# Performance work log

Hardware: AMD Instinct MI355X
Metric: run time of the kernel (lower is better)

## Reference

```python
import jax, jax.numpy as jnp
import numpy as np

D_MODEL, D_FF, N_EXPERTS, TOP_K = 1024, 4096, 8, 2


def setup_inputs() -> dict:
    key = jax.random.key(0)
    ks = jax.random.split(key, 7)
    s = 0.02
    return {
        "x": jax.random.normal(ks[0], (2, 2048, D_MODEL), dtype=jnp.float32),
        "router_w": jax.random.normal(ks[1], (D_MODEL, N_EXPERTS), dtype=jnp.float32) * s,
        "router_b": jnp.zeros((N_EXPERTS,), dtype=jnp.float32),
        "w1": jax.random.normal(ks[2], (N_EXPERTS, D_MODEL, D_FF), dtype=jnp.float32) * s,
        "b1": jnp.zeros((N_EXPERTS, D_FF), dtype=jnp.float32),
        "w2": jax.random.normal(ks[3], (N_EXPERTS, D_FF, D_MODEL), dtype=jnp.float32) * s,
        "b2": jnp.zeros((N_EXPERTS, D_MODEL), dtype=jnp.float32),
    }


def reference(x, router_w, router_b, w1, b1, w2, b2):
    bsz, seq_len, d_model = x.shape
    flat_x = x.reshape(-1, d_model)                      # [T, D]
    logits = flat_x @ router_w + router_b                # [T, E]
    topk_scores, topk_idx = jax.lax.top_k(logits, TOP_K) # [T, K]
    gates = jax.nn.softmax(topk_scores, axis=-1).astype(flat_x.dtype)
    mixed = jnp.zeros_like(flat_x)
    num_experts = w1.shape[0]
    for e in range(num_experts):
        # dense per-expert MLP over all tokens; tokens not routed to e get weight 0,
        # so the math matches the original gather-MLP-scatter exactly.
        h = jax.nn.gelu(flat_x @ w1[e] + b1[e], approximate=False)  # exact GELU as torch nn.GELU
        y = h @ w2[e] + b2[e]                                       # [T, D]
        w_e = jnp.sum(jnp.where(topk_idx == e, gates, 0.0), axis=-1, keepdims=True)  # [T, 1]
        mixed = mixed + w_e * y
    return mixed.reshape(bsz, seq_len, d_model)
```

## Files before the change

kernel.cpp:

```cpp
#include <hip/hip_runtime.h>
#include <hip/hip_bf16.h>
#include <stdint.h>

#define T_TOK 4096
#define DM 1024
#define DF 4096
#define NE 8
#define PADROWS 9216

typedef __attribute__((ext_vector_type(8))) short short8;
typedef __attribute__((ext_vector_type(8))) unsigned short ushort8_t;
typedef __attribute__((ext_vector_type(4))) float f32x4;

__device__ __forceinline__ unsigned short f2bf(float f) {
    union { float f; unsigned u; } v; v.f = f;
    unsigned r = v.u + 0x7fffu + ((v.u >> 16) & 1u);
    return (unsigned short)(r >> 16);
}

__device__ __forceinline__ void async_cp16(const void* g, void* l) {
    __builtin_amdgcn_global_load_lds(
        (const __attribute__((address_space(1))) unsigned*)g,
        (__attribute__((address_space(3))) unsigned*)l,
        16, 0, 0);
}

__global__ __launch_bounds__(256) void k_router(
    const float* __restrict__ x, const float* __restrict__ rw,
    const float* __restrict__ rb, int* __restrict__ counts,
    int* __restrict__ listTok, float* __restrict__ listGate)
{
    int l  = threadIdx.x & 63;
    int wv = threadIdx.x >> 6;
    int t  = blockIdx.x * 4 + wv;
    const float* xr = x + (size_t)t * DM;
    float acc[NE];
#pragma unroll
    for (int e = 0; e < NE; ++e) acc[e] = 0.f;
#pragma unroll
    for (int i = 0; i < 16; ++i) {
        int d = i * 64 + l;
        float xv = xr[d];
        const float4* wp = (const float4*)(rw + (size_t)d * NE);
        float4 w0 = wp[0], w1 = wp[1];
        acc[0] += xv * w0.x; acc[1] += xv * w0.y; acc[2] += xv * w0.z; acc[3] += xv * w0.w;
        acc[4] += xv * w1.x; acc[5] += xv * w1.y; acc[6] += xv * w1.z; acc[7] += xv * w1.w;
    }
#pragma unroll
    for (int off = 32; off >= 1; off >>= 1)
#pragma unroll
        for (int e = 0; e < NE; ++e) acc[e] += __shfl_down(acc[e], off);
    if (l == 0) {
        float lg[NE];
#pragma unroll
        for (int e = 0; e < NE; ++e) lg[e] = acc[e] + rb[e];
        int i1 = 0; float s1 = lg[0];
#pragma unroll
        for (int e = 1; e < NE; ++e) if (lg[e] > s1) { s1 = lg[e]; i1 = e; }
        int i2 = -1; float s2 = -3.0e38f;
#pragma unroll
        for (int e = 0; e < NE; ++e) if (e != i1 && lg[e] > s2) { s2 = lg[e]; i2 = e; }
        float g1 = 1.f / (1.f + expf(s2 - s1));
        float g2 = 1.f - g1;
        int p1 = atomicAdd(&counts[i1], 1);
        listTok[i1 * T_TOK + p1] = t; listGate[i1 * T_TOK + p1] = g1;
        int p2 = atomicAdd(&counts[i2], 1);
        listTok[i2 * T_TOK + p2] = t; listGate[i2 * T_TOK + p2] = g2;
    }
}

__global__ void k_offsets(const int* __restrict__ counts, int* __restrict__ offsets)
{
    int cum = 0;
    for (int e = 0; e < NE; ++e) { offsets[e] = cum; cum += (counts[e] + 127) & ~127; }
    offsets[NE] = cum;
}

__global__ __launch_bounds__(256) void k_packw(const float* __restrict__ src,
                                               unsigned short* __restrict__ dst,
                                               int K, int N)
{
    __shared__ float tile[64][65];
    int e  = blockIdx.z;
    int n0 = blockIdx.x * 64;
    int k0 = blockIdx.y * 64;
    const float* s    = src + (size_t)e * K * N;
    unsigned short* d = dst + (size_t)e * K * N;
    int tid = threadIdx.x;
#pragma unroll
    for (int i = 0; i < 4; ++i) {
        int u  = i * 256 + tid;
        int kk = u >> 4;
        int nn = (u & 15) * 4;
        float4 v = *(const float4*)(s + (size_t)(k0 + kk) * N + n0 + nn);
        tile[kk][nn] = v.x; tile[kk][nn + 1] = v.y; tile[kk][nn + 2] = v.z; tile[kk][nn + 3] = v.w;
    }
    __syncthreads();
#pragma unroll
    for (int i = 0; i < 4; ++i) {
        int u  = i * 256 + tid;
        int nn = u >> 4;
        int g  = (u >> 1) & 7;
        int h  = (u & 1) * 4;
        int kc = g * 8 + h;
        int n  = n0 + nn;
        ushort4 o;
        o.x = f2bf(tile[kc + 0][nn]); o.y = f2bf(tile[kc + 1][nn]);
        o.z = f2bf(tile[kc + 2][nn]); o.w = f2bf(tile[kc + 3][nn]);
        int gp = g ^ (n & 7);
        size_t off = ((size_t)(k0 >> 6) * N + n) * 64 + gp * 8 + h;
        *(ushort4*)(d + off) = o;
    }
}

__global__ __launch_bounds__(256) void k_packa(
    const float* __restrict__ x, const int* __restrict__ listTok,
    const int* __restrict__ counts, const int* __restrict__ offsets,
    unsigned short* __restrict__ ap)
{
    int r0  = blockIdx.x * 64;
    int kt  = blockIdx.y;
    int tid = threadIdx.x;
    __shared__ int toks[64];
    if (tid < 64) {
        int r = r0 + tid;
        int tok = 0;
        int total = offsets[NE];
        if (r < total) {
            int e = 0;
#pragma unroll
            for (int j = 1; j < NE; ++j) if (r >= offsets[j]) e = j;
            int local = r - offsets[e];
            int c = counts[e];
            if (local >= c) local = c - 1;
            if (local < 0) local = 0;
            tok = listTok[e * T_TOK + local];
        }
        toks[tid] = tok;
    }
    __syncthreads();
#pragma unroll
    for (int i = 0; i < 4; ++i) {
        int u  = i * 256 + tid;
        int rl = u >> 4;
        int g  = (u >> 1) & 7;
        int h  = (u & 1) * 4;
        int tok = toks[rl];
        float4 v = *(const float4*)(x + (size_t)tok * DM + kt * 64 + g * 8 + h);
        ushort4 o; o.x = f2bf(v.x); o.y = f2bf(v.y); o.z = f2bf(v.z); o.w = f2bf(v.w);
        int row = r0 + rl;
        int gp  = g ^ (row & 7);
        size_t off = ((size_t)kt * PADROWS + row) * 64 + gp * 8 + h;
        *(ushort4*)(ap + off) = o;
    }
}

__global__ __launch_bounds__(256) void k_ffn1(
    const unsigned short* __restrict__ ap, const unsigned short* __restrict__ w1p,
    const float* __restrict__ b1, const int* __restrict__ counts,
    const int* __restrict__ offsets, unsigned short* __restrict__ Hp)
{
    __shared__ __align__(16) unsigned short lsA[128 * 64];
    __shared__ __align__(16) unsigned short lsB[128 * 64];
    int i  = blockIdx.x;
    int l0 = ((i & 7) << 10) + (i >> 3);
    int xx = l0 & 255, y = l0 >> 8;
    int e = xx >> 5, mt = xx & 31;
    int cnt = counts[e];
    int m0  = mt << 7;
    if (m0 >= cnt) return;
    int hbase = offsets[e];
    int n0    = y << 7;
    int tid = threadIdx.x, wv = tid >> 6, l = tid & 63;
    int wm = wv & 1, wn = wv >> 1;

    const unsigned short* srcA = ap + ((size_t)hbase + m0) * 64;
    const unsigned short* srcB = w1p + (size_t)e * DM * DF;

    f32x4 acc[4][4];
#pragma unroll
    for (int a = 0; a < 4; ++a)
#pragma unroll
        for (int b = 0; b < 4; ++b) acc[a][b] = (f32x4)(0.f);

    for (int kt = 0; kt < 16; ++kt) {
        const unsigned short* gA = srcA + (size_t)kt * PADROWS * 64;
        const unsigned short* gB = srcB + ((size_t)kt * DF + n0) * 64;
#pragma unroll
        for (int j = 0; j < 4; ++j) {
            int c = (wv * 4 + j) * 512;
            async_cp16(gA + c + l * 8, lsA + c);
            async_cp16(gB + c + l * 8, lsB + c);
        }
        __syncthreads();
#pragma unroll
        for (int ks = 0; ks < 2; ++ks) {
            short8 aF[4], bF[4];
#pragma unroll
            for (int mi = 0; mi < 4; ++mi) {
                int row = wm * 64 + mi * 16 + (l & 15);
                int g   = ks * 4 + (l >> 4);
                aF[mi] = *(const short8*)&lsA[row * 64 + ((g ^ (row & 7)) << 3)];
            }
#pragma unroll
            for (int ni = 0; ni < 4; ++ni) {
                int row = wn * 64 + ni * 16 + (l & 15);
                int g   = ks * 4 + (l >> 4);
                bF[ni] = *(const short8*)&lsB[row * 64 + ((g ^ (row & 7)) << 3)];
            }
#pragma unroll
            for (int mi = 0; mi < 4; ++mi)
#pragma unroll
                for (int ni = 0; ni < 4; ++ni)
                    acc[mi][ni] = __builtin_amdgcn_mfma_f32_16x16x32_bf16(aF[mi], bF[ni], acc[mi][ni], 0, 0, 0);
        }
        __syncthreads();
    }

    int q = l >> 4, cn = l & 15;
#pragma unroll
    for (int mi = 0; mi < 4; ++mi) {
#pragma unroll
        for (int ni = 0; ni < 4; ++ni) {
            int nloc = wn * 64 + ni * 16 + cn;
            float bias = b1[e * DF + n0 + nloc];
            unsigned short* base = (nloc & 64) ? lsB : lsA;
            int kc = nloc & 63, g = kc >> 3;
#pragma unroll
            for (int rg = 0; rg < 4; ++rg) {
                int m = wm * 64 + mi * 16 + q * 4 + rg;
                float v = acc[mi][ni][rg] + bias;
                v = 0.5f * v * (1.f + erff(v * 0.70710678118f));
                int gp = g ^ (m & 7);
                base[m * 64 + gp * 8 + (kc & 7)] = f2bf(v);
            }
        }
    }
    __syncthreads();
    {
        int c = tid >> 7;
        int r = tid & 127;
        const unsigned short* s = (c ? lsB : lsA) + r * 64;
        unsigned short* dst = Hp + (((size_t)(n0 >> 6) + c) * PADROWS + hbase + m0 + r) * 64;
#pragma unroll
        for (int j = 0; j < 8; ++j)
            *(ushort8_t*)(dst + j * 8) = *(const ushort8_t*)(s + j * 8);
    }
}

__global__ __launch_bounds__(256) void k_ffn2(
    const unsigned short* __restrict__ Hp, const unsigned short* __restrict__ w2p,
    const float* __restrict__ b2, const int* __restrict__ listTok,
    const float* __restrict__ listGate, const int* __restrict__ counts,
    const int* __restrict__ offsets, float* __restrict__ out)
{
    __shared__ __align__(16) unsigned short lsA[128 * 64];
    __shared__ __align__(16) unsigned short lsB[128 * 64];
    int i  = blockIdx.x;
    int l0 = ((i & 7) << 8) + (i >> 3);
    int xx = l0 & 255, y = l0 >> 8;
    int e = xx >> 5, mt = xx & 31;
    int cnt = counts[e];
    int m0  = mt << 7;
    if (m0 >= cnt) return;
    int hbase = offsets[e];
    int n0    = y << 7;
    int tid = threadIdx.x, wv = tid >> 6, l = tid & 63;
    int wm = wv & 1, wn = wv >> 1;

    const unsigned short* srcA = Hp + ((size_t)hbase + m0) * 64;
    const unsigned short* srcB = w2p + (size_t)e * DF * DM;

    f32x4 acc[4][4];
#pragma unroll
    for (int a = 0; a < 4; ++a)
#pragma unroll
        for (int b = 0; b < 4; ++b) acc[a][b] = (f32x4)(0.f);

    for (int kt = 0; kt < 64; ++kt) {
        const unsigned short* gA = srcA + (size_t)kt * PADROWS * 64;
        const unsigned short* gB = srcB + ((size_t)kt * DM + n0) * 64;
#pragma unroll
        for (int j = 0; j < 4; ++j) {
            int c = (wv * 4 + j) * 512;
            async_cp16(gA + c + l * 8, lsA + c);
            async_cp16(gB + c + l * 8, lsB + c);
        }
        __syncthreads();
#pragma unroll
        for (int ks = 0; ks < 2; ++ks) {
            short8 aF[4], bF[4];
#pragma unroll
            for (int mi = 0; mi < 4; ++mi) {
                int row = wm * 64 + mi * 16 + (l & 15);
                int g   = ks * 4 + (l >> 4);
                aF[mi] = *(const short8*)&lsA[row * 64 + ((g ^ (row & 7)) << 3)];
            }
#pragma unroll
            for (int ni = 0; ni < 4; ++ni) {
                int row = wn * 64 + ni * 16 + (l & 15);
                int g   = ks * 4 + (l >> 4);
                bF[ni] = *(const short8*)&lsB[row * 64 + ((g ^ (row & 7)) << 3)];
            }
#pragma unroll
            for (int mi = 0; mi < 4; ++mi)
#pragma unroll
                for (int ni = 0; ni < 4; ++ni)
                    acc[mi][ni] = __builtin_amdgcn_mfma_f32_16x16x32_bf16(aF[mi], bF[ni], acc[mi][ni], 0, 0, 0);
        }
        __syncthreads();
    }

    int q = l >> 4, cn = l & 15;
    const int*   lt  = listTok  + e * T_TOK;
    const float* lgt = listGate + e * T_TOK;
#pragma unroll
    for (int mi = 0; mi < 4; ++mi) {
#pragma unroll
        for (int rg = 0; rg < 4; ++rg) {
            int m = wm * 64 + mi * 16 + q * 4 + rg;
            int r = m0 + m;
            if (r < cnt) {
                int tok = lt[r];
                float ggt = lgt[r];
                float* orow = out + (size_t)tok * DM;
#pragma unroll
                for (int ni = 0; ni < 4; ++ni) {
                    int n = n0 + wn * 64 + ni * 16 + cn;
                    float v = acc[mi][ni][rg] + b2[e * DM + n];
                    atomicAdd(&orow[n], ggt * v);
                }
            }
        }
    }
}

extern "C" void kernel_launch(void* const* d_in, const int* in_sizes, int n_in,
                              void* d_out, int out_size, void* d_ws, size_t ws_size,
                              hipStream_t stream)
{
    const float* x  = (const float*)d_in[0];
    const float* rw = (const float*)d_in[1];
    const float* rb = (const float*)d_in[2];
    const float* w1 = (const float*)d_in[3];
    const float* b1 = (const float*)d_in[4];
    const float* w2 = (const float*)d_in[5];
    const float* b2 = (const float*)d_in[6];
    float* out = (float*)d_out;

    char* ws = (char*)d_ws;
    int*            counts   = (int*)(ws + 0);
    int*            offsets  = (int*)(ws + 128);
    int*            listTok  = (int*)(ws + 512);
    float*          listGate = (float*)(ws + 512 + 131072);
    unsigned short* apack    = (unsigned short*)(ws + 262656);
    unsigned short* w2p      = (unsigned short*)(ws + 262656);
    unsigned short* w1p      = (unsigned short*)(ws + 19137024);
    unsigned short* Hp       = (unsigned short*)(ws + 86245888);

    hipMemsetAsync(counts, 0, 32, stream);
    hipMemsetAsync(d_out, 0, (size_t)out_size * sizeof(float), stream);

    k_router <<<T_TOK / 4, 256, 0, stream>>>(x, rw, rb, counts, listTok, listGate);
    k_offsets<<<1, 1, 0, stream>>>(counts, offsets);
    k_packw  <<<dim3(DF / 64, DM / 64, NE), 256, 0, stream>>>(w1, w1p, DM, DF);
    k_packa  <<<dim3(PADROWS / 64, 16), 256, 0, stream>>>(x, listTok, counts, offsets, apack);
    k_ffn1   <<<NE * 32 * 32, 256, 0, stream>>>(apack, w1p, b1, counts, offsets, Hp);
    k_packw  <<<dim3(DM / 64, DF / 64, NE), 256, 0, stream>>>(w2, w2p, DF, DM);
    k_ffn2   <<<NE * 32 * 8, 256, 0, stream>>>(Hp, w2p, b2, listTok, listGate, counts, offsets, out);
}
```

Baseline: 697.4 us.

## Rework MoE GEMMs with 4-stage async pipeline, bigger tiles, atomic-free combine

Both expert GEMMs switch to 32-wide K slabs with a new XOR swizzle, 512-thread blocks and a 4-deep async global-to-LDS pipeline using explicit vmcnt waits and raw barriers. FFN1 grows its tile to 256x256 and FFN2 to 256x128, with MFMA priority raised during compute. The FFN2 epilogue writes per-row outputs to a workspace buffer instead of atomically adding into the output. A new gather kernel then combines each token's two expert rows with the gate weights, which removes the output memset and the atomics. This costs an extra fp32 intermediate buffer and a larger LDS footprint, and row padding grows to 256.

```diff
diff --git a/kernel.cpp b/kernel.cpp
--- a/kernel.cpp
+++ b/kernel.cpp
@@ -6,7 +6,7 @@
 #define DM 1024
 #define DF 4096
 #define NE 8
-#define PADROWS 9216
+#define PADROWS 10240
 
 typedef __attribute__((ext_vector_type(8))) short short8;
 typedef __attribute__((ext_vector_type(8))) unsigned short ushort8_t;
@@ -25,10 +25,17 @@
         16, 0, 0);
 }
 
+#define WAITV(n)  asm volatile("s_waitcnt vmcnt(" #n ")" ::: "memory")
+#define WAITLGKM() asm volatile("s_waitcnt lgkmcnt(0)" ::: "memory")
+#define BAR()     asm volatile("s_barrier" ::: "memory")
+
+__device__ __forceinline__ int swz(int g, int r) { return g ^ (r & 3) ^ ((r >> 2) & 3); }
+
 __global__ __launch_bounds__(256) void k_router(
     const float* __restrict__ x, const float* __restrict__ rw,
     const float* __restrict__ rb, int* __restrict__ counts,
-    int* __restrict__ listTok, float* __restrict__ listGate)
+    int* __restrict__ listTok, int4* __restrict__ tokRec,
+    float2* __restrict__ tokGate)
 {
     int l  = threadIdx.x & 63;
     int wv = threadIdx.x >> 6;
@@ -63,16 +70,18 @@
         float g1 = 1.f / (1.f + expf(s2 - s1));
         float g2 = 1.f - g1;
         int p1 = atomicAdd(&counts[i1], 1);
-        listTok[i1 * T_TOK + p1] = t; listGate[i1 * T_TOK + p1] = g1;
+        listTok[i1 * T_TOK + p1] = t;
         int p2 = atomicAdd(&counts[i2], 1);
-        listTok[i2 * T_TOK + p2] = t; listGate[i2 * T_TOK + p2] = g2;
+        listTok[i2 * T_TOK + p2] = t;
+        tokRec[t]  = make_int4(i1, p1, i2, p2);
+        tokGate[t] = make_float2(g1, g2);
     }
 }
 
 __global__ void k_offsets(const int* __restrict__ counts, int* __restrict__ offsets)
 {
     int cum = 0;
-    for (int e = 0; e < NE; ++e) { offsets[e] = cum; cum += (counts[e] + 127) & ~127; }
+    for (int e = 0; e < NE; ++e) { offsets[e] = cum; cum += (counts[e] + 255) & ~255; }
     offsets[NE] = cum;
 }
 
@@ -97,19 +106,17 @@
     }
     __syncthreads();
 #pragma unroll
-    for (int i = 0; i < 4; ++i) {
+    for (int i = 0; i < 2; ++i) {
         int u  = i * 256 + tid;
-        int nn = u >> 4;
-        int g  = (u >> 1) & 7;
-        int h  = (u & 1) * 4;
-        int kc = g * 8 + h;
+        int nn = u >> 3;
+        int kg = u & 7;
+        int gg = kg & 3;
         int n  = n0 + nn;
-        ushort4 o;
-        o.x = f2bf(tile[kc + 0][nn]); o.y = f2bf(tile[kc + 1][nn]);
-        o.z = f2bf(tile[kc + 2][nn]); o.w = f2bf(tile[kc + 3][nn]);
-        int gp = g ^ (n & 7);
-        size_t off = ((size_t)(k0 >> 6) * N + n) * 64 + gp * 8 + h;
-        *(ushort4*)(d + off) = o;
+        ushort8_t o;
+#pragma unroll
+        for (int j = 0; j < 8; ++j) o[j] = f2bf(tile[kg * 8 + j][nn]);
+        size_t slab = (size_t)(k0 >> 5) + (kg >> 2);
+        *(ushort8_t*)(d + (slab * N + n) * 32 + (swz(gg, n) << 3)) = o;
     }
 }
 
@@ -118,9 +125,9 @@
     const int* __restrict__ counts, const int* __restrict__ offsets,
     unsigned short* __restrict__ ap)
 {
-    int r0  = blockIdx.x * 64;
-    int kt  = blockIdx.y;
-    int tid = threadIdx.x;
+    int r0   = blockIdx.x * 64;
+    int slab = blockIdx.y;
+    int tid  = threadIdx.x;
     __shared__ int toks[64];
     if (tid < 64) {
         int r = r0 + tid;
@@ -134,142 +141,157 @@
             int c = counts[e];
             if (local >= c) local = c - 1;
             if (local < 0) local = 0;
-            tok = listTok[e * T_TOK + local];
+            tok = (c > 0) ? listTok[e * T_TOK + local] : 0;
         }
         toks[tid] = tok;
     }
     __syncthreads();
-#pragma unroll
-    for (int i = 0; i < 4; ++i) {
-        int u  = i * 256 + tid;
-        int rl = u >> 4;
-        int g  = (u >> 1) & 7;
-        int h  = (u & 1) * 4;
-        int tok = toks[rl];
-        float4 v = *(const float4*)(x + (size_t)tok * DM + kt * 64 + g * 8 + h);
-        ushort4 o; o.x = f2bf(v.x); o.y = f2bf(v.y); o.z = f2bf(v.z); o.w = f2bf(v.w);
-        int row = r0 + rl;
-        int gp  = g ^ (row & 7);
-        size_t off = ((size_t)kt * PADROWS + row) * 64 + gp * 8 + h;
-        *(ushort4*)(ap + off) = o;
-    }
-}
-
-__global__ __launch_bounds__(256) void k_ffn1(
+    int rl = tid >> 2, gg = tid & 3;
+    int tok = toks[rl];
+    const float4* src = (const float4*)(x + (size_t)tok * DM + slab * 32 + gg * 8);
+    float4 v0 = src[0], v1 = src[1];
+    ushort8_t o;
+    o[0] = f2bf(v0.x); o[1] = f2bf(v0.y); o[2] = f2bf(v0.z); o[3] = f2bf(v0.w);
+    o[4] = f2bf(v1.x); o[5] = f2bf(v1.y); o[6] = f2bf(v1.z); o[7] = f2bf(v1.w);
+    int rr = r0 + rl;
+    *(ushort8_t*)(ap + ((size_t)slab * PADROWS + rr) * 32 + (swz(gg, rr) << 3)) = o;
+}
+
+__global__ __launch_bounds__(512, 2) void k_ffn1(
     const unsigned short* __restrict__ ap, const unsigned short* __restrict__ w1p,
     const float* __restrict__ b1, const int* __restrict__ counts,
     const int* __restrict__ offsets, unsigned short* __restrict__ Hp)
 {
-    __shared__ __align__(16) unsigned short lsA[128 * 64];
-    __shared__ __align__(16) unsigned short lsB[128 * 64];
-    int i  = blockIdx.x;
-    int l0 = ((i & 7) << 10) + (i >> 3);
-    int xx = l0 & 255, y = l0 >> 8;
-    int e = xx >> 5, mt = xx & 31;
+    __shared__ __align__(16) unsigned short lds[65536];
+    int i = blockIdx.x;
+    int L = (i & 7) * 256 + (i >> 3);
+    int mt = L & 15, grp = L >> 4;
+    int y = grp & 15, e = grp >> 4;
     int cnt = counts[e];
-    int m0  = mt << 7;
+    int m0  = mt << 8;
     if (m0 >= cnt) return;
-    int hbase = offsets[e];
-    int n0    = y << 7;
+    int R0 = offsets[e] + m0;
+    int n0 = y << 8;
+
     int tid = threadIdx.x, wv = tid >> 6, l = tid & 63;
-    int wm = wv & 1, wn = wv >> 1;
-
-    const unsigned short* srcA = ap + ((size_t)hbase + m0) * 64;
-    const unsigned short* srcB = w1p + (size_t)e * DM * DF;
-
-    f32x4 acc[4][4];
-#pragma unroll
-    for (int a = 0; a < 4; ++a)
+    int wm = wv >> 2, wn = wv & 3;
+    int g = l >> 4, lr = l & 15;
+
+    int offA[8], offB[4];
+#pragma unroll
+    for (int mi = 0; mi < 8; ++mi) {
+        int r = wm * 128 + mi * 16 + lr;
+        offA[mi] = r * 32 + (swz(g, r) << 3);
+    }
+#pragma unroll
+    for (int ni = 0; ni < 4; ++ni) {
+        int r = wn * 64 + ni * 16 + lr;
+        offB[ni] = 8192 + r * 32 + (swz(g, r) << 3);
+    }
+
+    const unsigned short* gA = ap + (size_t)R0 * 32;
+    const unsigned short* gB = w1p + (size_t)e * DM * DF + (size_t)n0 * 32;
+
+    f32x4 acc[8][4];
+#pragma unroll
+    for (int a = 0; a < 8; ++a)
 #pragma unroll
         for (int b = 0; b < 4; ++b) acc[a][b] = (f32x4)(0.f);
 
-    for (int kt = 0; kt < 16; ++kt) {
-        const unsigned short* gA = srcA + (size_t)kt * PADROWS * 64;
-        const unsigned short* gB = srcB + ((size_t)kt * DF + n0) * 64;
-#pragma unroll
-        for (int j = 0; j < 4; ++j) {
-            int c = (wv * 4 + j) * 512;
-            async_cp16(gA + c + l * 8, lsA + c);
-            async_cp16(gB + c + l * 8, lsB + c);
-        }
-        __syncthreads();
-#pragma unroll
-        for (int ks = 0; ks < 2; ++ks) {
-            short8 aF[4], bF[4];
-#pragma unroll
-            for (int mi = 0; mi < 4; ++mi) {
-                int row = wm * 64 + mi * 16 + (l & 15);
-                int g   = ks * 4 + (l >> 4);
-                aF[mi] = *(const short8*)&lsA[row * 64 + ((g ^ (row & 7)) << 3)];
-            }
-#pragma unroll
-            for (int ni = 0; ni < 4; ++ni) {
-                int row = wn * 64 + ni * 16 + (l & 15);
-                int g   = ks * 4 + (l >> 4);
-                bF[ni] = *(const short8*)&lsB[row * 64 + ((g ^ (row & 7)) << 3)];
-            }
-#pragma unroll
-            for (int mi = 0; mi < 4; ++mi)
-#pragma unroll
-                for (int ni = 0; ni < 4; ++ni)
-                    acc[mi][ni] = __builtin_amdgcn_mfma_f32_16x16x32_bf16(aF[mi], bF[ni], acc[mi][ni], 0, 0, 0);
-        }
-        __syncthreads();
-    }
-
-    int q = l >> 4, cn = l & 15;
-#pragma unroll
-    for (int mi = 0; mi < 4; ++mi) {
-#pragma unroll
-        for (int ni = 0; ni < 4; ++ni) {
-            int nloc = wn * 64 + ni * 16 + cn;
-            float bias = b1[e * DF + n0 + nloc];
-            unsigned short* base = (nloc & 64) ? lsB : lsA;
-            int kc = nloc & 63, g = kc >> 3;
+#define STAGE1(t) { \
+    unsigned short* sb = lds + (((t) & 3) << 14); \
+    const unsigned short* ga = gA + (size_t)(t) * (PADROWS * 32); \
+    const unsigned short* gb = gB + (size_t)(t) * (DF * 32); \
+    int c0 = wv * 512; \
+    async_cp16(ga + c0 + l * 8,        sb + c0); \
+    async_cp16(ga + 4096 + c0 + l * 8, sb + 4096 + c0); \
+    async_cp16(gb + c0 + l * 8,        sb + 8192 + c0); \
+    async_cp16(gb + 4096 + c0 + l * 8, sb + 12288 + c0); }
+
+#define COMPUTE1(t) { \
+    const unsigned short* sb = lds + (((t) & 3) << 14); \
+    short8 aF[8], bF[4]; \
+    _Pragma("unroll") for (int ni = 0; ni < 4; ++ni) bF[ni] = *(const short8*)(sb + offB[ni]); \
+    _Pragma("unroll") for (int mi = 0; mi < 8; ++mi) aF[mi] = *(const short8*)(sb + offA[mi]); \
+    __builtin_amdgcn_s_setprio(1); \
+    _Pragma("unroll") for (int mi = 0; mi < 8; ++mi) \
+    _Pragma("unroll") for (int ni = 0; ni < 4; ++ni) \
+        acc[mi][ni] = __builtin_amdgcn_mfma_f32_16x16x32_bf16(aF[mi], bF[ni], acc[mi][ni], 0, 0, 0); \
+    __builtin_amdgcn_s_setprio(0); }
+
+    STAGE1(0); STAGE1(1); STAGE1(2);
+    for (int t = 0; t < 29; ++t) {
+        STAGE1(t + 3);
+        WAITV(12); BAR();
+        COMPUTE1(t);
+        BAR();
+    }
+    WAITV(8); BAR(); COMPUTE1(29); BAR();
+    WAITV(4); BAR(); COMPUTE1(30); BAR();
+    WAITV(0); BAR(); COMPUTE1(31); BAR();
+
+#pragma unroll
+    for (int ni = 0; ni < 4; ++ni) {
+        int nloc = wn * 64 + ni * 16 + lr;
+        float bias = b1[e * DF + n0 + nloc];
+        int slab = nloc >> 5, c = nloc & 31, g2 = c >> 3;
+#pragma unroll
+        for (int mi = 0; mi < 8; ++mi) {
 #pragma unroll
             for (int rg = 0; rg < 4; ++rg) {
-                int m = wm * 64 + mi * 16 + q * 4 + rg;
+                int m = wm * 128 + mi * 16 + g * 4 + rg;
                 float v = acc[mi][ni][rg] + bias;
                 v = 0.5f * v * (1.f + erff(v * 0.70710678118f));
-                int gp = g ^ (m & 7);
-                base[m * 64 + gp * 8 + (kc & 7)] = f2bf(v);
+                lds[(slab << 13) + m * 32 + (swz(g2, m) << 3) + (c & 7)] = f2bf(v);
             }
         }
     }
-    __syncthreads();
-    {
-        int c = tid >> 7;
-        int r = tid & 127;
-        const unsigned short* s = (c ? lsB : lsA) + r * 64;
-        unsigned short* dst = Hp + (((size_t)(n0 >> 6) + c) * PADROWS + hbase + m0 + r) * 64;
-#pragma unroll
-        for (int j = 0; j < 8; ++j)
-            *(ushort8_t*)(dst + j * 8) = *(const ushort8_t*)(s + j * 8);
-    }
-}
-
-__global__ __launch_bounds__(256) void k_ffn2(
+    WAITLGKM(); BAR();
+#pragma unroll
+    for (int j = 0; j < 16; ++j) {
+        int u = j * 512 + tid;
+        int elem = u * 8;
+        int slab = elem >> 13;
+        int rem  = elem & 8191;
+        *(ushort8_t*)(Hp + ((size_t)((n0 >> 5) + slab) * PADROWS + R0) * 32 + rem) =
+            *(const ushort8_t*)(lds + elem);
+    }
+}
+
+__global__ __launch_bounds__(512, 2) void k_ffn2(
     const unsigned short* __restrict__ Hp, const unsigned short* __restrict__ w2p,
-    const float* __restrict__ b2, const int* __restrict__ listTok,
-    const float* __restrict__ listGate, const int* __restrict__ counts,
-    const int* __restrict__ offsets, float* __restrict__ out)
-{
-    __shared__ __align__(16) unsigned short lsA[128 * 64];
-    __shared__ __align__(16) unsigned short lsB[128 * 64];
-    int i  = blockIdx.x;
-    int l0 = ((i & 7) << 8) + (i >> 3);
-    int xx = l0 & 255, y = l0 >> 8;
-    int e = xx >> 5, mt = xx & 31;
+    const float* __restrict__ b2, const int* __restrict__ counts,
+    const int* __restrict__ offsets, float* __restrict__ ypart)
+{
+    __shared__ __align__(16) unsigned short lds[49152];
+    int i = blockIdx.x;
+    int L = (i & 7) * 128 + (i >> 3);
+    int mt = L & 15, grp = L >> 4;
+    int y = grp & 7, e = grp >> 3;
     int cnt = counts[e];
-    int m0  = mt << 7;
+    int m0  = mt << 8;
     if (m0 >= cnt) return;
-    int hbase = offsets[e];
-    int n0    = y << 7;
+    int R0 = offsets[e] + m0;
+    int n0 = y << 7;
+
     int tid = threadIdx.x, wv = tid >> 6, l = tid & 63;
-    int wm = wv & 1, wn = wv >> 1;
-
-    const unsigned short* srcA = Hp + ((size_t)hbase + m0) * 64;
-    const unsigned short* srcB = w2p + (size_t)e * DF * DM;
+    int wm = wv >> 1, wn = wv & 1;
+    int g = l >> 4, lr = l & 15;
+
+    int offA[4], offB[4];
+#pragma unroll
+    for (int mi = 0; mi < 4; ++mi) {
+        int r = wm * 64 + mi * 16 + lr;
+        offA[mi] = r * 32 + (swz(g, r) << 3);
+    }
+#pragma unroll
+    for (int ni = 0; ni < 4; ++ni) {
+        int r = wn * 64 + ni * 16 + lr;
+        offB[ni] = 8192 + r * 32 + (swz(g, r) << 3);
+    }
+
+    const unsigned short* gA = Hp + (size_t)R0 * 32;
+    const unsigned short* gB = w2p + (size_t)e * DF * DM + (size_t)n0 * 32;
 
     f32x4 acc[4][4];
 #pragma unroll
@@ -277,62 +299,73 @@
 #pragma unroll
         for (int b = 0; b < 4; ++b) acc[a][b] = (f32x4)(0.f);
 
-    for (int kt = 0; kt < 64; ++kt) {
-        const unsigned short* gA = srcA + (size_t)kt * PADROWS * 64;
-        const unsigned short* gB = srcB + ((size_t)kt * DM + n0) * 64;
-#pragma unroll
-        for (int j = 0; j < 4; ++j) {
-            int c = (wv * 4 + j) * 512;
-            async_cp16(gA + c + l * 8, lsA + c);
-            async_cp16(gB + c + l * 8, lsB + c);
-        }
-        __syncthreads();
-#pragma unroll
-        for (int ks = 0; ks < 2; ++ks) {
-            short8 aF[4], bF[4];
-#pragma unroll
-            for (int mi = 0; mi < 4; ++mi) {
-                int row = wm * 64 + mi * 16 + (l & 15);
-                int g   = ks * 4 + (l >> 4);
-                aF[mi] = *(const short8*)&lsA[row * 64 + ((g ^ (row & 7)) << 3)];
-            }
+#define STAGE2(t) { \
+    unsigned short* sb = lds + ((t) & 3) * 12288; \
+    const unsigned short* ga = gA + (size_t)(t) * (PADROWS * 32); \
+    const unsigned short* gb = gB + (size_t)(t) * (DM * 32); \
+    int c0 = wv * 512; \
+    async_cp16(ga + c0 + l * 8,        sb + c0); \
+    async_cp16(ga + 4096 + c0 + l * 8, sb + 4096 + c0); \
+    async_cp16(gb + c0 + l * 8,        sb + 8192 + c0); }
+
+#define COMPUTE2(t) { \
+    const unsigned short* sb = lds + ((t) & 3) * 12288; \
+    short8 aF[4], bF[4]; \
+    _Pragma("unroll") for (int ni = 0; ni < 4; ++ni) bF[ni] = *(const short8*)(sb + offB[ni]); \
+    _Pragma("unroll") for (int mi = 0; mi < 4; ++mi) aF[mi] = *(const short8*)(sb + offA[mi]); \
+    __builtin_amdgcn_s_setprio(1); \
+    _Pragma("unroll") for (int mi = 0; mi < 4; ++mi) \
+    _Pragma("unroll") for (int ni = 0; ni < 4; ++ni) \
+        acc[mi][ni] = __builtin_amdgcn_mfma_f32_16x16x32_bf16(aF[mi], bF[ni], acc[mi][ni], 0, 0, 0); \
+    __builtin_amdgcn_s_setprio(0); }
+
+    STAGE2(0); STAGE2(1); STAGE2(2);
+    for (int t = 0; t < 125; ++t) {
+        STAGE2(t + 3);
+        WAITV(9); BAR();
+        COMPUTE2(t);
+        BAR();
+    }
+    WAITV(6); BAR(); COMPUTE2(125); BAR();
+    WAITV(3); BAR(); COMPUTE2(126); BAR();
+    WAITV(0); BAR(); COMPUTE2(127); BAR();
+
+    float bias[4];
+#pragma unroll
+    for (int ni = 0; ni < 4; ++ni) bias[ni] = b2[e * DM + n0 + wn * 64 + ni * 16 + lr];
+#pragma unroll
+    for (int mi = 0; mi < 4; ++mi) {
+#pragma unroll
+        for (int rg = 0; rg < 4; ++rg) {
+            int m = wm * 64 + mi * 16 + g * 4 + rg;
+            size_t row = (size_t)R0 + m;
 #pragma unroll
             for (int ni = 0; ni < 4; ++ni) {
-                int row = wn * 64 + ni * 16 + (l & 15);
-                int g   = ks * 4 + (l >> 4);
-                bF[ni] = *(const short8*)&lsB[row * 64 + ((g ^ (row & 7)) << 3)];
-            }
-#pragma unroll
-            for (int mi = 0; mi < 4; ++mi)
-#pragma unroll
-                for (int ni = 0; ni < 4; ++ni)
-                    acc[mi][ni] = __builtin_amdgcn_mfma_f32_16x16x32_bf16(aF[mi], bF[ni], acc[mi][ni], 0, 0, 0);
-        }
-        __syncthreads();
-    }
-
-    int q = l >> 4, cn = l & 15;
-    const int*   lt  = listTok  + e * T_TOK;
-    const float* lgt = listGate + e * T_TOK;
-#pragma unroll
-    for (int mi = 0; mi < 4; ++mi) {
-#pragma unroll
-        for (int rg = 0; rg < 4; ++rg) {
-            int m = wm * 64 + mi * 16 + q * 4 + rg;
-            int r = m0 + m;
-            if (r < cnt) {
-                int tok = lt[r];
-                float ggt = lgt[r];
-                float* orow = out + (size_t)tok * DM;
-#pragma unroll
-                for (int ni = 0; ni < 4; ++ni) {
-                    int n = n0 + wn * 64 + ni * 16 + cn;
-                    float v = acc[mi][ni][rg] + b2[e * DM + n];
-                    atomicAdd(&orow[n], ggt * v);
-                }
+                ypart[row * DM + n0 + wn * 64 + ni * 16 + lr] = acc[mi][ni][rg] + bias[ni];
             }
         }
     }
+}
+
+__global__ __launch_bounds__(256) void k_gather(
+    const float* __restrict__ yp, const int4* __restrict__ rec,
+    const float2* __restrict__ gg, const int* __restrict__ offsets,
+    float* __restrict__ out)
+{
+    int t = blockIdx.x;
+    int4 rc = rec[t];
+    float2 w = gg[t];
+    size_t r1 = (size_t)offsets[rc.x] + rc.y;
+    size_t r2 = (size_t)offsets[rc.z] + rc.w;
+    const float4* a = (const float4*)(yp + r1 * DM);
+    const float4* b = (const float4*)(yp + r2 * DM);
+    float4 va = a[threadIdx.x], vb = b[threadIdx.x];
+    float4 o;
+    o.x = w.x * va.x + w.y * vb.x;
+    o.y = w.x * va.y + w.y * vb.y;
+    o.z = w.x * va.z + w.y * vb.z;
+    o.w = w.x * va.w + w.y * vb.w;
+    ((float4*)(out + (size_t)t * DM))[threadIdx.x] = o;
 }
 
 extern "C" void kernel_launch(void* const* d_in, const int* in_sizes, int n_in,
@@ -352,20 +385,22 @@
     int*            counts   = (int*)(ws + 0);
     int*            offsets  = (int*)(ws + 128);
     int*            listTok  = (int*)(ws + 512);
-    float*          listGate = (float*)(ws + 512 + 131072);
     unsigned short* apack    = (unsigned short*)(ws + 262656);
     unsigned short* w2p      = (unsigned short*)(ws + 262656);
-    unsigned short* w1p      = (unsigned short*)(ws + 19137024);
-    unsigned short* Hp       = (unsigned short*)(ws + 86245888);
+    unsigned short* w1p      = (unsigned short*)(ws + 21234176);
+    unsigned short* Hp       = (unsigned short*)(ws + 88343040);
+    float*          ypart    = (float*)(ws + 172229120);
+    int4*           tokRec   = (int4*)(ws + 214172160);
+    float2*         tokGate  = (float2*)(ws + 214237696);
 
     hipMemsetAsync(counts, 0, 32, stream);
-    hipMemsetAsync(d_out, 0, (size_t)out_size * sizeof(float), stream);
-
-    k_router <<<T_TOK / 4, 256, 0, stream>>>(x, rw, rb, counts, listTok, listGate);
+
+    k_router <<<T_TOK / 4, 256, 0, stream>>>(x, rw, rb, counts, listTok, tokRec, tokGate);
     k_offsets<<<1, 1, 0, stream>>>(counts, offsets);
     k_packw  <<<dim3(DF / 64, DM / 64, NE), 256, 0, stream>>>(w1, w1p, DM, DF);
-    k_packa  <<<dim3(PADROWS / 64, 16), 256, 0, stream>>>(x, listTok, counts, offsets, apack);
-    k_ffn1   <<<NE * 32 * 32, 256, 0, stream>>>(apack, w1p, b1, counts, offsets, Hp);
+    k_packa  <<<dim3(PADROWS / 64, 32), 256, 0, stream>>>(x, listTok, counts, offsets, apack);
+    k_ffn1   <<<2048, 512, 0, stream>>>(apack, w1p, b1, counts, offsets, Hp);
     k_packw  <<<dim3(DM / 64, DF / 64, NE), 256, 0, stream>>>(w2, w2p, DF, DM);
-    k_ffn2   <<<NE * 32 * 8, 256, 0, stream>>>(Hp, w2p, b2, listTok, listGate, counts, offsets, out);
-}
+    k_ffn2   <<<1024, 512, 0, stream>>>(Hp, w2p, b2, counts, offsets, ypart);
+    k_gather <<<T_TOK, 256, 0, stream>>>(ypart, tokRec, tokGate, offsets, out);
+}
```

Result: slower. 755.4 us (+8.3%).
